# Kernel optimization log

Hardware: AMD Instinct MI355X
Metric: run time of the kernel (lower is better)

The kernel has to match this reference:

```python
import jax, jax.numpy as jnp
import numpy as np

HEADS = 8
DIM_HEAD = 64
DIM = 512
EPS = 1e-7  # module's self.eps, also used as LayerNorm eps


def _per_head_layernorm(t, w, b):
    # t: [b, h, n, d]; w, b: [h, d] (one LayerNorm per head, affine)
    mu = t.mean(axis=-1, keepdims=True)
    var = t.var(axis=-1, keepdims=True)  # biased, matches torch LayerNorm
    tn = (t - mu) * jax.lax.rsqrt(var + EPS)
    return tn * w[None, :, None, :] + b[None, :, None, :]


def setup_inputs() -> dict:
    key = jax.random.key(0)
    ks = jax.random.split(key, 4)
    inner = HEADS * DIM_HEAD
    return {
        "x": jax.random.normal(ks[0], (2, 2048, DIM), dtype=jnp.float32),
        "w_qkv": jax.random.normal(ks[1], (3 * inner, DIM), dtype=jnp.float32) * 0.02,
        "lnk_w": jnp.ones((HEADS, DIM_HEAD), dtype=jnp.float32),
        "lnk_b": jnp.zeros((HEADS, DIM_HEAD), dtype=jnp.float32),
        "lnv_w": jnp.ones((HEADS, DIM_HEAD), dtype=jnp.float32),
        "lnv_b": jnp.zeros((HEADS, DIM_HEAD), dtype=jnp.float32),
        "w_out": jax.random.normal(ks[2], (DIM, inner), dtype=jnp.float32) * 0.02,
        "b_out": jnp.zeros((DIM,), dtype=jnp.float32),
    }


def reference(x, w_qkv, lnk_w, lnk_b, lnv_w, lnv_b, w_out, b_out):
    b, n, _ = x.shape
    qkv = x @ w_qkv.T  # [b, n, 3*inner]
    q, k, v = jnp.split(qkv, 3, axis=-1)

    def split_heads(t):  # [b, n, h*d] -> [b, h, n, d]
        return t.reshape(b, n, HEADS, DIM_HEAD).transpose(0, 2, 1, 3)

    q, k, v = map(split_heads, (q, k, v))

    # per-head LayerNorm over dim_head on k and v
    k = _per_head_layernorm(k, lnk_w, lnk_b)
    v = _per_head_layernorm(v, lnv_w, lnv_b)

    # causal linear attention: prefix sums of k and of k-v outer products
    k_cum = jnp.cumsum(k, axis=2)  # [b, h, n, d]
    # scores: [b, h, n, d, e] prefix sums of outer products, scaled by 1/seq_len
    scores = jnp.cumsum(jnp.einsum('bhnd,bhne->bhnde', k, v), axis=2) / n
    d_inv = 1.0 / jnp.einsum('bhnd,bhnd->bhn', k_cum + EPS, q)  # [b, h, n]
    out = jnp.einsum('bhnd,bhnde,bhn->bhne', q, scores, d_inv)  # [b, h, n, e]

    out = out.transpose(0, 2, 1, 3).reshape(b, n, HEADS * DIM_HEAD)  # b n (h e)
    return out @ w_out.T + b_out
```

## Files before the change

kernel.cpp:

```cpp
#include <hip/hip_runtime.h>

constexpr int Bb   = 2;
constexpr int Nn   = 2048;
constexpr int Hh   = 8;
constexpr int Dd   = 64;
constexpr int Mm   = Bb * Nn;
constexpr int TQKV = 1536;
constexpr int INNER = Hh * Dd;
constexpr int CH   = 64;
constexpr int NCH  = Nn / CH;
constexpr int CSZ  = Dd * Dd + Dd;
constexpr float EPSF = 1e-7f;

typedef _Float16 half8 __attribute__((ext_vector_type(8)));
typedef _Float16 half4 __attribute__((ext_vector_type(4)));
typedef float f32x4 __attribute__((ext_vector_type(4)));

#define AS1(p) ((const __attribute__((address_space(1))) unsigned int*)(p))
#define AS3(p) ((__attribute__((address_space(3))) unsigned int*)(p))

__global__ __launch_bounds__(128) void gemm1_f32(
    const float* __restrict__ A, const float* __restrict__ B,
    float* __restrict__ C) {
  __shared__ float As[32][68];
  __shared__ float Bs[32][68];
  const int tid = threadIdx.x;
  const int tx = tid & 15, ty = tid >> 4;
  const int bm = blockIdx.y * 64, bn = blockIdx.x * 64;
  const int row = tid & 63, c4base = tid >> 6;

  float acc[8][4] = {};

  for (int k0 = 0; k0 < 512; k0 += 32) {
#pragma unroll
    for (int p = 0; p < 4; ++p) {
      int c4 = c4base + 2 * p;
      float4 fa = *(const float4*)(A + (size_t)(bm + row) * 512 + k0 + c4 * 4);
      As[c4 * 4 + 0][row] = fa.x; As[c4 * 4 + 1][row] = fa.y;
      As[c4 * 4 + 2][row] = fa.z; As[c4 * 4 + 3][row] = fa.w;
      float4 fb = *(const float4*)(B + (size_t)(bn + row) * 512 + k0 + c4 * 4);
      Bs[c4 * 4 + 0][row] = fb.x; Bs[c4 * 4 + 1][row] = fb.y;
      Bs[c4 * 4 + 2][row] = fb.z; Bs[c4 * 4 + 3][row] = fb.w;
    }
    __syncthreads();
#pragma unroll
    for (int kk = 0; kk < 32; ++kk) {
      float a[8], b[4];
      *(float4*)&a[0] = *(const float4*)&As[kk][ty * 8];
      *(float4*)&a[4] = *(const float4*)&As[kk][ty * 8 + 4];
      *(float4*)&b[0] = *(const float4*)&Bs[kk][tx * 4];
#pragma unroll
      for (int i = 0; i < 8; ++i)
#pragma unroll
        for (int j = 0; j < 4; ++j) acc[i][j] += a[i] * b[j];
    }
    __syncthreads();
  }

#pragma unroll
  for (int i = 0; i < 8; ++i) {
    size_t r = bm + ty * 8 + i;
    float4 v;
    v.x = acc[i][0]; v.y = acc[i][1]; v.z = acc[i][2]; v.w = acc[i][3];
    *(float4*)(C + r * (size_t)TQKV + bn + tx * 4) = v;
  }
}

__global__ __launch_bounds__(256) void split_f16_k(
    const float* __restrict__ s, _Float16* __restrict__ hi,
    _Float16* __restrict__ lo, int n4) {
  int i = blockIdx.x * 256 + threadIdx.x;
  if (i >= n4) return;
  float4 a = ((const float4*)s)[i];
  half4 h, l;
  float av[4] = {a.x, a.y, a.z, a.w};
#pragma unroll
  for (int j = 0; j < 4; ++j) {
    _Float16 hh = (_Float16)av[j];
    h[j] = hh;
    l[j] = (_Float16)((av[j] - (float)hh) * 2048.0f);
  }
  ((half4*)hi)[i] = h;
  ((half4*)lo)[i] = l;
}

__global__ __launch_bounds__(256) void gemm_split_nt(
    const _Float16* __restrict__ Ah, const _Float16* __restrict__ Al,
    const _Float16* __restrict__ Bh, const _Float16* __restrict__ Bl,
    const float* __restrict__ bias, float* __restrict__ C,
    int Ndim, int Kd) {
  constexpr int BM = 128, BN = 64, BK = 32;
  __shared__ _Float16 lds[(2 * BM + 2 * BN) * BK];
  constexpr int AHo = 0;
  constexpr int ALo = BM * BK;
  constexpr int BHo = 2 * BM * BK;
  constexpr int BLo = 2 * BM * BK + BN * BK;

  const int tid = threadIdx.x;
  const int wave = tid >> 6, lane = tid & 63;
  const int lq = lane >> 4, lm = lane & 15;
  const int bm = blockIdx.y * BM, bn = blockIdx.x * BN;

  f32x4 acc[2][4] = {};
  f32x4 corr[2][4] = {};

  const int nsteps = Kd >> 5;
  for (int ks = 0; ks < nsteps; ++ks) {
    const int k0 = ks * BK;
    for (int idx = wave; idx < 24; idx += 4) {
      int t, j;
      if (idx < 8)       { t = 0; j = idx; }
      else if (idx < 16) { t = 1; j = idx - 8; }
      else if (idx < 20) { t = 2; j = idx - 16; }
      else               { t = 3; j = idx - 20; }
      const int row = j * 16 + (lane >> 2);
      const _Float16* g;
      _Float16* l;
      if (t == 0)      { g = Ah + (size_t)(bm + row) * Kd; l = lds + AHo + j * 16 * BK; }
      else if (t == 1) { g = Al + (size_t)(bm + row) * Kd; l = lds + ALo + j * 16 * BK; }
      else if (t == 2) { g = Bh + (size_t)(bn + row) * Kd; l = lds + BHo + j * 16 * BK; }
      else             { g = Bl + (size_t)(bn + row) * Kd; l = lds + BLo + j * 16 * BK; }
      g += k0 + (lane & 3) * 8;
      __builtin_amdgcn_global_load_lds(AS1(g), AS3(l), 16, 0, 0);
    }
    __syncthreads();

    half8 ahf[2], alf[2], bhf[4], blf[4];
    const int mwo = wave * 32;
#pragma unroll
    for (int fi = 0; fi < 2; ++fi) {
      ahf[fi] = *(const half8*)&lds[AHo + (mwo + fi * 16 + lm) * BK + lq * 8];
      alf[fi] = *(const half8*)&lds[ALo + (mwo + fi * 16 + lm) * BK + lq * 8];
    }
#pragma unroll
    for (int fj = 0; fj < 4; ++fj) {
      bhf[fj] = *(const half8*)&lds[BHo + (fj * 16 + lm) * BK + lq * 8];
      blf[fj] = *(const half8*)&lds[BLo + (fj * 16 + lm) * BK + lq * 8];
    }
#pragma unroll
    for (int fi = 0; fi < 2; ++fi)
#pragma unroll
      for (int fj = 0; fj < 4; ++fj) {
        acc[fi][fj] = __builtin_amdgcn_mfma_f32_16x16x32_f16(
            ahf[fi], bhf[fj], acc[fi][fj], 0, 0, 0);
        corr[fi][fj] = __builtin_amdgcn_mfma_f32_16x16x32_f16(
            ahf[fi], blf[fj], corr[fi][fj], 0, 0, 0);
        corr[fi][fj] = __builtin_amdgcn_mfma_f32_16x16x32_f16(
            alf[fi], bhf[fj], corr[fi][fj], 0, 0, 0);
      }
    __syncthreads();
  }

#pragma unroll
  for (int fi = 0; fi < 2; ++fi) {
    const int m0 = bm + wave * 32 + fi * 16 + lq * 4;
#pragma unroll
    for (int fj = 0; fj < 4; ++fj) {
      const int n = bn + fj * 16 + lm;
      const float bb = bias ? bias[n] : 0.f;
      f32x4 v = acc[fi][fj];
      f32x4 cv = corr[fi][fj];
#pragma unroll
      for (int r = 0; r < 4; ++r)
        C[(size_t)(m0 + r) * Ndim + n] = v[r] + cv[r] * (1.0f / 2048.0f) + bb;
    }
  }
}

__global__ __launch_bounds__(256) void chunk_sums_ln(
    float* __restrict__ qkv, const float* __restrict__ lnk_w,
    const float* __restrict__ lnk_b, const float* __restrict__ lnv_w,
    const float* __restrict__ lnv_b, float* __restrict__ cbuf) {
  int blk = blockIdx.x;
  int c = blk % NCH;
  int bh = blk / NCH;
  int h = bh % Hh, b = bh / Hh;
  __shared__ float Ks[CH][68];
  __shared__ float Vs[CH][68];
  int tid = threadIdx.x;
  float* base = qkv + (size_t)(b * Nn + c * CH) * TQKV + h * Dd;
  for (int i = tid; i < CH * 16; i += 256) {
    int row = i >> 4, c4 = i & 15;
    *(float4*)&Ks[row][c4 * 4] =
        *(const float4*)(base + (size_t)row * TQKV + INNER + c4 * 4);
    *(float4*)&Vs[row][c4 * 4] =
        *(const float4*)(base + (size_t)row * TQKV + 2 * INNER + c4 * 4);
  }
  __syncthreads();

  if (tid < 128) {
    bool isv = tid >= 64;
    int row = tid & 63;
    float* R = isv ? &Vs[row][0] : &Ks[row][0];
    float s = 0.f, s2 = 0.f;
#pragma unroll
    for (int j = 0; j < 64; j += 4) {
      float4 v = *(const float4*)&R[j];
      s += v.x + v.y + v.z + v.w;
      s2 += v.x * v.x + v.y * v.y + v.z * v.z + v.w * v.w;
    }
    float mean = s * (1.f / 64.f);
    float var = s2 * (1.f / 64.f) - mean * mean;
    float inv = 1.0f / sqrtf(var + EPSF);
    const float* w = isv ? lnv_w : lnk_w;
    const float* bb = isv ? lnv_b : lnk_b;
#pragma unroll
    for (int j = 0; j < 64; ++j)
      R[j] = (R[j] - mean) * inv * w[h * Dd + j] + bb[h * Dd + j];
  }
  __syncthreads();

  for (int i = tid; i < CH * 16; i += 256) {
    int row = i >> 4, c4 = i & 15;
    *(float4*)(base + (size_t)row * TQKV + INNER + c4 * 4) =
        *(const float4*)&Ks[row][c4 * 4];
    *(float4*)(base + (size_t)row * TQKV + 2 * INNER + c4 * 4) =
        *(const float4*)&Vs[row][c4 * 4];
  }

  int d0 = (tid >> 4) * 4, e0 = (tid & 15) * 4;
  float acc[4][4] = {};
  float kc[4] = {0.f, 0.f, 0.f, 0.f};
  for (int n = 0; n < CH; ++n) {
    float4 kv = *(const float4*)&Ks[n][d0];
    float4 vv = *(const float4*)&Vs[n][e0];
    float ka[4] = {kv.x, kv.y, kv.z, kv.w};
    float va[4] = {vv.x, vv.y, vv.z, vv.w};
#pragma unroll
    for (int i = 0; i < 4; ++i)
#pragma unroll
      for (int j = 0; j < 4; ++j) acc[i][j] += ka[i] * va[j];
    if (e0 == 0) {
#pragma unroll
      for (int i = 0; i < 4; ++i) kc[i] += ka[i];
    }
  }
  float* out = cbuf + (size_t)blk * CSZ;
#pragma unroll
  for (int i = 0; i < 4; ++i) {
    float4 r;
    r.x = acc[i][0]; r.y = acc[i][1]; r.z = acc[i][2]; r.w = acc[i][3];
    *(float4*)(out + (size_t)(d0 + i) * Dd + e0) = r;
  }
  if (e0 == 0) {
#pragma unroll
    for (int i = 0; i < 4; ++i) out[Dd * Dd + d0 + i] = kc[i];
  }
}

__global__ __launch_bounds__(256) void chunk_prefix(float* __restrict__ cbuf) {
  int bh = blockIdx.y;
  int i = blockIdx.x * 256 + threadIdx.x;
  if (i >= CSZ) return;
  float* p = cbuf + (size_t)bh * NCH * CSZ + i;
  float carry = 0.f;
  for (int c = 0; c < NCH; ++c) {
    float t = p[(size_t)c * CSZ];
    p[(size_t)c * CSZ] = carry;
    carry += t;
  }
}

__global__ __launch_bounds__(256) void chunk_attn(
    const float* __restrict__ qkv, const float* __restrict__ cbuf,
    _Float16* __restrict__ atth, _Float16* __restrict__ attl) {
  int blk = blockIdx.x;
  int c = blk % NCH;
  int bh = blk / NCH;
  int h = bh % Hh, b = bh / Hh;
  __shared__ float Qs[64][68];
  __shared__ float Ks[64][68];
  __shared__ float Vs[64][68];
  __shared__ float Ss[64][68];
  __shared__ float kcs[64];
  __shared__ float rs[64][17];
  __shared__ float denomS[64];
  float (*Ps)[68] = Ks;

  int tid = threadIdx.x;
  int tx = tid & 15, ty = tid >> 4;
  const float* base = qkv + (size_t)(b * Nn + c * CH) * TQKV + h * Dd;
  for (int i = tid; i < CH * 16; i += 256) {
    int row = i >> 4, c4 = i & 15;
    float4 fq = *(const float4*)(base + (size_t)row * TQKV + c4 * 4);
    Qs[c4 * 4 + 0][row] = fq.x; Qs[c4 * 4 + 1][row] = fq.y;
    Qs[c4 * 4 + 2][row] = fq.z; Qs[c4 * 4 + 3][row] = fq.w;
    float4 fk = *(const float4*)(base + (size_t)row * TQKV + INNER + c4 * 4);
    Ks[c4 * 4 + 0][row] = fk.x; Ks[c4 * 4 + 1][row] = fk.y;
    Ks[c4 * 4 + 2][row] = fk.z; Ks[c4 * 4 + 3][row] = fk.w;
    float4 fv = *(const float4*)(base + (size_t)row * TQKV + 2 * INNER + c4 * 4);
    *(float4*)&Vs[row][c4 * 4] = fv;
  }
  const float* sp = cbuf + (size_t)blk * CSZ;
  for (int i = tid; i < 1024; i += 256) {
    int row = i >> 4;
    *(float4*)&Ss[row][(i & 15) * 4] = *(const float4*)(sp + (size_t)i * 4);
  }
  if (tid < 16) {
    float4 f = *(const float4*)(sp + Dd * Dd + tid * 4);
    kcs[tid * 4 + 0] = f.x; kcs[tid * 4 + 1] = f.y;
    kcs[tid * 4 + 2] = f.z; kcs[tid * 4 + 3] = f.w;
  }
  __syncthreads();

  float accP[4][4] = {};
  for (int kk = 0; kk < 64; ++kk) {
    float4 qa = *(const float4*)&Qs[kk][ty * 4];
    float4 kb = *(const float4*)&Ks[kk][tx * 4];
    float qv[4] = {qa.x, qa.y, qa.z, qa.w};
    float kv[4] = {kb.x, kb.y, kb.z, kb.w};
#pragma unroll
    for (int i = 0; i < 4; ++i)
#pragma unroll
      for (int j = 0; j < 4; ++j) accP[i][j] += qv[i] * kv[j];
  }
  __syncthreads();

#pragma unroll
  for (int i = 0; i < 4; ++i) {
    int n = ty * 4 + i;
    float rsum = 0.f;
#pragma unroll
    for (int j = 0; j < 4; ++j) {
      int m = tx * 4 + j;
      float p = (m <= n) ? accP[i][j] : 0.f;
      Ps[m][n] = p;
      rsum += p;
    }
    rs[n][tx] = rsum;
  }
  __syncthreads();

  float accO[4][4] = {};
  for (int d = 0; d < 64; ++d) {
    float4 qa = *(const float4*)&Qs[d][ty * 4];
    float4 sb = *(const float4*)&Ss[d][tx * 4];
    float qv[4] = {qa.x, qa.y, qa.z, qa.w};
    float sv[4] = {sb.x, sb.y, sb.z, sb.w};
#pragma unroll
    for (int i = 0; i < 4; ++i)
#pragma unroll
      for (int j = 0; j < 4; ++j) accO[i][j] += qv[i] * sv[j];
  }
  if (tid < 64) {
    int n = tid;
    float qkc = 0.f, qs = 0.f;
    for (int d = 0; d < 64; ++d) {
      float q = Qs[d][n];
      qkc += q * kcs[d];
      qs += q;
    }
    float rsum = 0.f;
#pragma unroll
    for (int t2 = 0; t2 < 16; ++t2) rsum += rs[n][t2];
    denomS[n] = qkc + rsum + EPSF * qs;
  }
  __syncthreads();

  for (int m = 0; m < 64; ++m) {
    float4 pa = *(const float4*)&Ps[m][ty * 4];
    float4 vb = *(const float4*)&Vs[m][tx * 4];
    float pv[4] = {pa.x, pa.y, pa.z, pa.w};
    float vv[4] = {vb.x, vb.y, vb.z, vb.w};
#pragma unroll
    for (int i = 0; i < 4; ++i)
#pragma unroll
      for (int j = 0; j < 4; ++j) accO[i][j] += pv[i] * vv[j];
  }

  size_t obase = (size_t)(b * Nn + c * CH) * INNER + h * Dd;
#pragma unroll
  for (int i = 0; i < 4; ++i) {
    int n = ty * 4 + i;
    float dinv = 1.0f / denomS[n];
    float scale = dinv * (1.0f / (float)Nn);
    half4 hv, lv;
#pragma unroll
    for (int j = 0; j < 4; ++j) {
      float o = accO[i][j] * scale;
      _Float16 hh = (_Float16)o;
      hv[j] = hh;
      lv[j] = (_Float16)((o - (float)hh) * 2048.0f);
    }
    *(half4*)(atth + obase + (size_t)n * INNER + tx * 4) = hv;
    *(half4*)(attl + obase + (size_t)n * INNER + tx * 4) = lv;
  }
}

extern "C" void kernel_launch(void* const* d_in, const int* in_sizes, int n_in,
                              void* d_out, int out_size, void* d_ws,
                              size_t ws_size, hipStream_t stream) {
  const float* x     = (const float*)d_in[0];
  const float* w_qkv = (const float*)d_in[1];
  const float* lnk_w = (const float*)d_in[2];
  const float* lnk_b = (const float*)d_in[3];
  const float* lnv_w = (const float*)d_in[4];
  const float* lnv_b = (const float*)d_in[5];
  const float* w_out = (const float*)d_in[6];
  const float* b_out = (const float*)d_in[7];
  float* out = (float*)d_out;

  float* qkv  = (float*)d_ws;
  float* cbuf = qkv + (size_t)Mm * TQKV;
  _Float16* atth = (_Float16*)(cbuf + (size_t)Bb * Hh * NCH * CSZ);
  _Float16* attl = atth + (size_t)Mm * INNER;
  _Float16* woh  = attl + (size_t)Mm * INNER;
  _Float16* wol  = woh + (size_t)INNER * 512;

  gemm1_f32<<<dim3(TQKV / 64, Mm / 64), 128, 0, stream>>>(x, w_qkv, qkv);

  chunk_sums_ln<<<Bb * Hh * NCH, 256, 0, stream>>>(
      qkv, lnk_w, lnk_b, lnv_w, lnv_b, cbuf);

  chunk_prefix<<<dim3((CSZ + 255) / 256, Bb * Hh), 256, 0, stream>>>(cbuf);

  split_f16_k<<<256, 256, 0, stream>>>(w_out, woh, wol, INNER * 512 / 4);

  chunk_attn<<<Bb * Hh * NCH, 256, 0, stream>>>(qkv, cbuf, atth, attl);

  gemm_split_nt<<<dim3(INNER / 64, Mm / 128), 256, 0, stream>>>(
      atth, attl, woh, wol, b_out, out, INNER, 512);
}
```

Before: 238.2 us.

## Compute V projection via split-f16 MFMA GEMM and enlarge fp32 QK GEMM tile

The fp32 QKV projection now covers only the Q and K columns, using a larger 128x64 tile with 256 threads. The V columns are computed by the existing hi/lo fp16-split MFMA GEMM, writing straight into the qkv buffer. To feed it, x and the V slice of w_qkv are split into fp16 hi/lo pairs. The aim is to move part of the slow SIMT fp32 work onto matrix cores, at the cost of two extra split kernels, more memory traffic, and some precision loss in V relative to pure fp32.

```diff
diff --git a/kernel.cpp b/kernel.cpp
--- a/kernel.cpp
+++ b/kernel.cpp
@@ -19,28 +19,33 @@
 #define AS1(p) ((const __attribute__((address_space(1))) unsigned int*)(p))
 #define AS3(p) ((__attribute__((address_space(3))) unsigned int*)(p))
 
-__global__ __launch_bounds__(128) void gemm1_f32(
+__global__ __launch_bounds__(256) void gemm1_f32(
     const float* __restrict__ A, const float* __restrict__ B,
     float* __restrict__ C) {
-  __shared__ float As[32][68];
+  __shared__ float As[32][132];
   __shared__ float Bs[32][68];
   const int tid = threadIdx.x;
   const int tx = tid & 15, ty = tid >> 4;
-  const int bm = blockIdx.y * 64, bn = blockIdx.x * 64;
-  const int row = tid & 63, c4base = tid >> 6;
+  const int bm = blockIdx.y * 128, bn = blockIdx.x * 64;
+  const int rowA = tid & 127, c4a = tid >> 7;
+  const int rowB = tid & 63,  c4b = tid >> 6;
 
   float acc[8][4] = {};
 
   for (int k0 = 0; k0 < 512; k0 += 32) {
 #pragma unroll
     for (int p = 0; p < 4; ++p) {
-      int c4 = c4base + 2 * p;
-      float4 fa = *(const float4*)(A + (size_t)(bm + row) * 512 + k0 + c4 * 4);
-      As[c4 * 4 + 0][row] = fa.x; As[c4 * 4 + 1][row] = fa.y;
-      As[c4 * 4 + 2][row] = fa.z; As[c4 * 4 + 3][row] = fa.w;
-      float4 fb = *(const float4*)(B + (size_t)(bn + row) * 512 + k0 + c4 * 4);
-      Bs[c4 * 4 + 0][row] = fb.x; Bs[c4 * 4 + 1][row] = fb.y;
-      Bs[c4 * 4 + 2][row] = fb.z; Bs[c4 * 4 + 3][row] = fb.w;
+      int c4 = c4a + 2 * p;
+      float4 fa = *(const float4*)(A + (size_t)(bm + rowA) * 512 + k0 + c4 * 4);
+      As[c4 * 4 + 0][rowA] = fa.x; As[c4 * 4 + 1][rowA] = fa.y;
+      As[c4 * 4 + 2][rowA] = fa.z; As[c4 * 4 + 3][rowA] = fa.w;
+    }
+#pragma unroll
+    for (int p = 0; p < 2; ++p) {
+      int c4 = c4b + 4 * p;
+      float4 fb = *(const float4*)(B + (size_t)(bn + rowB) * 512 + k0 + c4 * 4);
+      Bs[c4 * 4 + 0][rowB] = fb.x; Bs[c4 * 4 + 1][rowB] = fb.y;
+      Bs[c4 * 4 + 2][rowB] = fb.z; Bs[c4 * 4 + 3][rowB] = fb.w;
     }
     __syncthreads();
 #pragma unroll
@@ -59,10 +64,10 @@
 
 #pragma unroll
   for (int i = 0; i < 8; ++i) {
-    size_t r = bm + ty * 8 + i;
-    float4 v;
-    v.x = acc[i][0]; v.y = acc[i][1]; v.z = acc[i][2]; v.w = acc[i][3];
-    *(float4*)(C + r * (size_t)TQKV + bn + tx * 4) = v;
+    size_t row = bm + ty * 8 + i;
+    float4 r;
+    r.x = acc[i][0]; r.y = acc[i][1]; r.z = acc[i][2]; r.w = acc[i][3];
+    *(float4*)(C + row * (size_t)TQKV + bn + tx * 4) = r;
   }
 }
 
@@ -406,8 +411,19 @@
   _Float16* attl = atth + (size_t)Mm * INNER;
   _Float16* woh  = attl + (size_t)Mm * INNER;
   _Float16* wol  = woh + (size_t)INNER * 512;
-
-  gemm1_f32<<<dim3(TQKV / 64, Mm / 64), 128, 0, stream>>>(x, w_qkv, qkv);
+  _Float16* xh   = wol + (size_t)INNER * 512;
+  _Float16* xl   = xh + (size_t)Mm * 512;
+  _Float16* wvh  = xl + (size_t)Mm * 512;
+  _Float16* wvl  = wvh + (size_t)INNER * 512;
+
+  split_f16_k<<<2048, 256, 0, stream>>>(x, xh, xl, Mm * 512 / 4);
+  split_f16_k<<<256, 256, 0, stream>>>(
+      w_qkv + (size_t)1024 * 512, wvh, wvl, INNER * 512 / 4);
+
+  gemm1_f32<<<dim3(1024 / 64, Mm / 128), 256, 0, stream>>>(x, w_qkv, qkv);
+
+  gemm_split_nt<<<dim3(512 / 64, Mm / 128), 256, 0, stream>>>(
+      xh, xl, wvh, wvl, nullptr, qkv + 1024, TQKV, 512);
 
   chunk_sums_ln<<<Bb * Hh * NCH, 256, 0, stream>>>(
       qkv, lnk_w, lnk_b, lnv_w, lnv_b, cbuf);
```

After: 234.5 us. Within noise of the previous version (-1.5%).
